# Optimization experiments

Hardware: AMD Instinct MI355X
Metric: run time of the kernel (lower is better)

The kernel has to match this reference:

```python
import jax, jax.numpy as jnp
import numpy as np

N_NODES = 50000
NEG_SLOPE = 0.2


def gat_conv(x, src, dst, W, att_src, att_dst, bias, concat):
    # x: [N, F_in], W: [H*D, F_in], att_*: [H, D], bias: [H*D] or [D]
    N = x.shape[0]
    H, D = att_src.shape
    h = (x @ W.T).reshape(N, H, D)                      # [N, H, D]
    a_src = jnp.einsum('nhd,hd->nh', h, att_src)        # [N, H]
    a_dst = jnp.einsum('nhd,hd->nh', h, att_dst)        # [N, H]
    e = jax.nn.leaky_relu(a_src[src] + a_dst[dst], NEG_SLOPE)  # [E, H]
    # softmax over incoming edges of each destination node
    m = jax.ops.segment_max(e, dst, num_segments=N)     # [N, H]
    ex = jnp.exp(e - m[dst])
    denom = jax.ops.segment_sum(ex, dst, num_segments=N)
    alpha = ex / denom[dst]                             # [E, H]
    msg = alpha[:, :, None] * h[src]                    # [E, H, D]
    out = jax.ops.segment_sum(msg, dst, num_segments=N) # [N, H, D]
    out = out.reshape(N, H * D) if concat else out.mean(axis=1)
    return out + bias


def setup_inputs() -> dict:
    key = jax.random.key(0)
    ks = jax.random.split(key, 10)
    nfeat, nhid, nclass, heads = 256, 128, 40, 4
    d1 = nhid // heads  # 32
    E = 800000
    x = jax.random.normal(ks[0], (N_NODES, nfeat), dtype=jnp.float32)
    edge_index = jax.random.randint(ks[1], (2, E), 0, N_NODES, dtype=jnp.int64)
    s = 0.1
    W1 = jax.random.normal(ks[2], (heads * d1, nfeat), dtype=jnp.float32) * s
    att_src1 = jax.random.normal(ks[3], (heads, d1), dtype=jnp.float32) * s
    att_dst1 = jax.random.normal(ks[4], (heads, d1), dtype=jnp.float32) * s
    b1 = jnp.zeros((heads * d1,), dtype=jnp.float32)
    W2 = jax.random.normal(ks[5], (nclass, nhid), dtype=jnp.float32) * s
    att_src2 = jax.random.normal(ks[6], (1, nclass), dtype=jnp.float32) * s
    att_dst2 = jax.random.normal(ks[7], (1, nclass), dtype=jnp.float32) * s
    b2 = jnp.zeros((nclass,), dtype=jnp.float32)
    return {"x": x, "edge_index": edge_index, "W1": W1, "att_src1": att_src1,
            "att_dst1": att_dst1, "b1": b1, "W2": W2, "att_src2": att_src2,
            "att_dst2": att_dst2, "b2": b2}


def reference(x, edge_index, W1, att_src1, att_dst1, b1, W2, att_src2, att_dst2, b2):
    # PyG GATConv adds self-loops by default
    loops = jnp.arange(N_NODES, dtype=edge_index.dtype)
    src = jnp.concatenate([edge_index[0], loops])
    dst = jnp.concatenate([edge_index[1], loops])
    h = gat_conv(x, src, dst, W1, att_src1, att_dst1, b1, concat=True)
    h = jax.nn.relu(h)
    # dropout is identity in eval mode
    out = gat_conv(h, src, dst, W2, att_src2, att_dst2, b2, concat=True)
    return out
```

## Files before the change

### kernel.cpp

```cpp
#include <hip/hip_runtime.h>
#include <hip/hip_bf16.h>
#include <cstdint>
#include <cstddef>

#define N_NODES 50000
#define NEG_SLOPE 0.2f
#define NB 196
#define BIN_CHUNK 8192
#define SLICE_MAX 14336

typedef float floatx4 __attribute__((ext_vector_type(4)));
typedef short shortx8 __attribute__((ext_vector_type(8)));

__device__ __forceinline__ unsigned short f2b(float f) {
    union { float f; unsigned u; } v; v.f = f;
    unsigned u = v.u;
    return (unsigned short)((u + 0x7FFFu + ((u >> 16) & 1u)) >> 16);
}
__device__ __forceinline__ float b2f(unsigned short b) {
    union { unsigned u; float f; } v; v.u = ((unsigned)b) << 16;
    return v.f;
}

__global__ __launch_bounds__(256) void bucket_hist_kernel(
    const int* __restrict__ ei, int E0, int E, int* __restrict__ bhist) {
    __shared__ int h[NB];
    int t = threadIdx.x;
    for (int i = t; i < NB; i += 256) h[i] = 0;
    __syncthreads();
    int base = blockIdx.x * BIN_CHUNK;
    int end = min(base + BIN_CHUNK, E);
    for (int e = base + t; e < end; e += 256) {
        int d = (e < E0) ? ei[E0 + e] : (e - E0);
        atomicAdd(&h[d >> 8], 1);
    }
    __syncthreads();
    for (int i = t; i < NB; i += 256)
        if (h[i]) atomicAdd(&bhist[i], h[i]);
}

__global__ __launch_bounds__(256) void bucket_scan_kernel(
    const int* __restrict__ bhist, int* __restrict__ bbase,
    int* __restrict__ bcursor, int* __restrict__ rowptr, int E) {
    __shared__ int buf[256];
    int t = threadIdx.x;
    int v = (t < NB) ? bhist[t] : 0;
    int x = v;
    for (int off = 1; off < 256; off <<= 1) {
        buf[t] = x; __syncthreads();
        int y = (t >= off) ? buf[t - off] : 0;
        __syncthreads();
        x += y;
    }
    if (t < NB) {
        bbase[t] = x - v;
        bcursor[t] = x - v;
    }
    if (t == NB - 1) bbase[NB] = x;
    if (t == 0) rowptr[N_NODES] = E;
}

__global__ __launch_bounds__(256) void bin_kernel(
    const int* __restrict__ ei, int E0, int E,
    int* __restrict__ bcursor, unsigned int* __restrict__ ebuf) {
    __shared__ int h[NB];
    __shared__ int gbase[NB];
    int t = threadIdx.x;
    for (int i = t; i < NB; i += 256) h[i] = 0;
    __syncthreads();
    int base = blockIdx.x * BIN_CHUNK;
    int end = min(base + BIN_CHUNK, E);
    for (int e = base + t; e < end; e += 256) {
        int d = (e < E0) ? ei[E0 + e] : (e - E0);
        atomicAdd(&h[d >> 8], 1);
    }
    __syncthreads();
    for (int i = t; i < NB; i += 256) {
        int c = h[i];
        gbase[i] = c ? atomicAdd(&bcursor[i], c) : 0;
        h[i] = 0;
    }
    __syncthreads();
    for (int e = base + t; e < end; e += 256) {
        int s, d;
        if (e < E0) { s = ei[e]; d = ei[E0 + e]; }
        else        { s = e - E0; d = e - E0; }
        int b = d >> 8;
        int off = atomicAdd(&h[b], 1);
        ebuf[gbase[b] + off] = (unsigned)s | ((unsigned)(d & 255) << 16);
    }
}

__global__ __launch_bounds__(256) void build_kernel(
    const unsigned int* __restrict__ ebuf, const int* __restrict__ bbase,
    int* __restrict__ rowptr, int* __restrict__ csr_src) {
    __shared__ int h[256];
    __shared__ int lrp[257];
    __shared__ int stag[SLICE_MAX];
    int b = blockIdx.x, t = threadIdx.x;
    int e0 = bbase[b], e1 = bbase[b + 1];
    int cnt = e1 - e0;
    int n0 = b << 8;
    h[t] = 0;
    __syncthreads();
    for (int i = t; i < cnt; i += 256)
        atomicAdd(&h[ebuf[e0 + i] >> 16], 1);
    __syncthreads();
    int v = h[t], x = v;
    __shared__ int buf[256];
    for (int off = 1; off < 256; off <<= 1) {
        buf[t] = x; __syncthreads();
        int y = (t >= off) ? buf[t - off] : 0;
        __syncthreads();
        x += y;
    }
    lrp[t] = x - v;
    if (t == 255) lrp[256] = x;
    h[t] = 0;
    __syncthreads();
    int n = n0 + t;
    if (n < N_NODES) rowptr[n] = e0 + lrp[t];
    for (int i = t; i < cnt; i += 256) {
        unsigned int v2 = ebuf[e0 + i];
        int dloc = v2 >> 16;
        int off = atomicAdd(&h[dloc], 1);
        stag[lrp[dloc] + off] = (int)(v2 & 0xFFFFu);
    }
    __syncthreads();
    for (int i = t; i < cnt; i += 256) csr_src[e0 + i] = stag[i];
}

template <int BM, int BN, int NREAL, int KK, typename InT>
__global__ __launch_bounds__(256) void gemm_bf16_kernel(
    const InT* __restrict__ A, const float* __restrict__ B,
    unsigned short* __restrict__ Cb, int M) {
    const int BK = 64, LDK = 72;
    const int NT = BN / 16;
    __shared__ unsigned short As[BM * LDK];
    __shared__ unsigned short Bs[BN * LDK];
    const int t = threadIdx.x;
    const int wave = t >> 6, lane = t & 63;
    const int lrow = lane & 15, lkg = lane >> 4;
    const int bm = blockIdx.x * BM;

    floatx4 acc[NT] = {};

    for (int k0 = 0; k0 < KK; k0 += BK) {
        __syncthreads();
        if constexpr (sizeof(InT) == 4) {
            for (int i = t; i < BM * 16; i += 256) {
                int r = i >> 4, c4 = (i & 15) << 2;
                int gr = bm + r;
                float4 v = make_float4(0.f, 0.f, 0.f, 0.f);
                if (gr < M) v = *(const float4*)&A[(size_t)gr * KK + k0 + c4];
                int o = r * LDK + c4;
                As[o] = f2b(v.x); As[o + 1] = f2b(v.y);
                As[o + 2] = f2b(v.z); As[o + 3] = f2b(v.w);
            }
        } else {
            for (int i = t; i < BM * 8; i += 256) {
                int r = i >> 3, c8 = (i & 7) << 3;
                int gr = bm + r;
                shortx8 v = {};
                if (gr < M) v = *(const shortx8*)&A[(size_t)gr * KK + k0 + c8];
                *(shortx8*)&As[r * LDK + c8] = v;
            }
        }
        for (int i = t; i < BN * 16; i += 256) {
            int r = i >> 4, c4 = (i & 15) << 2;
            float4 v = make_float4(0.f, 0.f, 0.f, 0.f);
            if (r < NREAL) v = *(const float4*)&B[(size_t)r * KK + k0 + c4];
            int o = r * LDK + c4;
            Bs[o] = f2b(v.x); Bs[o + 1] = f2b(v.y);
            Bs[o + 2] = f2b(v.z); Bs[o + 3] = f2b(v.w);
        }
        __syncthreads();

        for (int ks = 0; ks < BK; ks += 32) {
            int kc = ks + lkg * 8;
            int row = wave * 16 + lrow;
            shortx8 a = *(const shortx8*)&As[row * LDK + kc];
#pragma unroll
            for (int nt = 0; nt < NT; nt++) {
                shortx8 b = *(const shortx8*)&Bs[(nt * 16 + lrow) * LDK + kc];
                acc[nt] = __builtin_amdgcn_mfma_f32_16x16x32_bf16(a, b, acc[nt], 0, 0, 0);
            }
        }
    }
#pragma unroll
    for (int nt = 0; nt < NT; nt++)
#pragma unroll
        for (int r = 0; r < 4; r++) {
            int row = bm + wave * 16 + lkg * 4 + r;
            int col = nt * 16 + lrow;
            if (row < M && col < NREAL)
                Cb[(size_t)row * NREAL + col] = f2b(acc[nt][r]);
        }
}

__global__ void att1_kernel(const unsigned short* __restrict__ h1b,
                            const float* __restrict__ att_src,
                            const float* __restrict__ att_dst,
                            float* __restrict__ a_src, float* __restrict__ a_dst,
                            int N) {
    int i = blockIdx.x * blockDim.x + threadIdx.x;
    if (i >= N * 4) return;
    int h = i & 3;
    const ushort4* hp = (const ushort4*)(h1b + (size_t)i * 32);
    const float4* as = (const float4*)(att_src + h * 32);
    const float4* ad = (const float4*)(att_dst + h * 32);
    float ssum = 0.f, dsum = 0.f;
#pragma unroll
    for (int j = 0; j < 8; j++) {
        ushort4 hv = hp[j];
        float4 av = as[j], dv = ad[j];
        float x0 = b2f(hv.x), x1 = b2f(hv.y), x2 = b2f(hv.z), x3 = b2f(hv.w);
        ssum += x0 * av.x + x1 * av.y + x2 * av.z + x3 * av.w;
        dsum += x0 * dv.x + x1 * dv.y + x2 * dv.z + x3 * dv.w;
    }
    a_src[i] = ssum;
    a_dst[i] = dsum;
}

__global__ void att2_kernel(const unsigned short* __restrict__ h2b,
                            const float* __restrict__ att_src,
                            const float* __restrict__ att_dst,
                            float* __restrict__ a_src, float* __restrict__ a_dst,
                            int N) {
    int n = blockIdx.x * blockDim.x + threadIdx.x;
    if (n >= N) return;
    const ushort4* hp = (const ushort4*)(h2b + (size_t)n * 40);
    const float4* as = (const float4*)att_src;
    const float4* ad = (const float4*)att_dst;
    float ssum = 0.f, dsum = 0.f;
#pragma unroll
    for (int j = 0; j < 10; j++) {
        ushort4 hv = hp[j];
        float4 av = as[j], dv = ad[j];
        float x0 = b2f(hv.x), x1 = b2f(hv.y), x2 = b2f(hv.z), x3 = b2f(hv.w);
        ssum += x0 * av.x + x1 * av.y + x2 * av.z + x3 * av.w;
        dsum += x0 * dv.x + x1 * dv.y + x2 * dv.z + x3 * dv.w;
    }
    a_src[n] = ssum;
    a_dst[n] = dsum;
}

__global__ __launch_bounds__(256) void agg1_kernel(
    const unsigned short* __restrict__ h1b, const float* __restrict__ a_src,
    const float* __restrict__ a_dst, const int* __restrict__ rowptr,
    const int* __restrict__ csr_src, const float* __restrict__ b1,
    unsigned short* __restrict__ zb, int N) {
    int wave = threadIdx.x >> 6, lane = threadIdx.x & 63;
    int n = blockIdx.x * 4 + wave;
    if (n >= N) return;
    int half = lane >> 5, pos = lane & 31, head = pos >> 3;
    float adn = a_dst[n * 4 + (lane & 3)];
    int beg = rowptr[n], deg = rowptr[n + 1] - beg;

    floatx4 acc = {0.f, 0.f, 0.f, 0.f};
    float den = 0.f;
    for (int c0 = 0; c0 < deg; c0 += 16) {
        int idx = c0 + (lane >> 2);
        int s_e = (idx < deg) ? csr_src[beg + idx] : 0;
        float l = a_src[(s_e << 2) + (lane & 3)] + adn;
        l = l > 0.f ? l : NEG_SLOPE * l;
        float w_e = __expf(l);
        int cnt = min(16, deg - c0);
#pragma unroll
        for (int e = 0; e < 16; e += 2) {
            int el = e + half;
            int s = __shfl(s_e, el << 2);
            float w = __shfl(w_e, (el << 2) + head);
            if (el < cnt) {
                ushort4 v = *(const ushort4*)&h1b[(size_t)s * 128 + pos * 4];
                den += w;
                acc.x += w * b2f(v.x); acc.y += w * b2f(v.y);
                acc.z += w * b2f(v.z); acc.w += w * b2f(v.w);
            }
        }
    }
    acc.x += __shfl_xor(acc.x, 32);
    acc.y += __shfl_xor(acc.y, 32);
    acc.z += __shfl_xor(acc.z, 32);
    acc.w += __shfl_xor(acc.w, 32);
    den   += __shfl_xor(den, 32);
    if (half == 0) {
        float inv = 1.f / den;
        float4 bb = *(const float4*)&b1[pos * 4];
        float o0 = fmaxf(acc.x * inv + bb.x, 0.f);
        float o1 = fmaxf(acc.y * inv + bb.y, 0.f);
        float o2 = fmaxf(acc.z * inv + bb.z, 0.f);
        float o3 = fmaxf(acc.w * inv + bb.w, 0.f);
        ushort4 r;
        r.x = f2b(o0); r.y = f2b(o1); r.z = f2b(o2); r.w = f2b(o3);
        *(ushort4*)&zb[(size_t)n * 128 + pos * 4] = r;
    }
}

__global__ __launch_bounds__(256) void agg2_kernel(
    const unsigned short* __restrict__ h2b, const float* __restrict__ a_src,
    const float* __restrict__ a_dst, const int* __restrict__ rowptr,
    const int* __restrict__ csr_src, const float* __restrict__ b2,
    float* __restrict__ out, int N) {
    int wave = threadIdx.x >> 6, lane = threadIdx.x & 63;
    int n = blockIdx.x * 4 + wave;
    if (n >= N) return;
    int half = lane >> 5, pos = lane & 31;
    float adn = a_dst[n];
    int beg = rowptr[n], deg = rowptr[n + 1] - beg;

    float2 acc = {0.f, 0.f};
    float den = 0.f;
    for (int c0 = 0; c0 < deg; c0 += 32) {
        int idx = c0 + lane;
        int s_e = (idx < deg) ? csr_src[beg + idx] : 0;
        float l = a_src[s_e] + adn;
        l = l > 0.f ? l : NEG_SLOPE * l;
        float w_e = __expf(l);
        int cnt = min(32, deg - c0);
#pragma unroll
        for (int e = 0; e < 32; e += 2) {
            int el = e + half;
            int s = __shfl(s_e, el);
            float w = __shfl(w_e, el);
            if (el < cnt) {
                den += w;
                if (pos < 20) {
                    ushort2 v = *(const ushort2*)&h2b[(size_t)s * 40 + pos * 2];
                    acc.x += w * b2f(v.x);
                    acc.y += w * b2f(v.y);
                }
            }
        }
    }
    acc.x += __shfl_xor(acc.x, 32);
    acc.y += __shfl_xor(acc.y, 32);
    den   += __shfl_xor(den, 32);
    if (half == 0 && pos < 20) {
        float inv = 1.f / den;
        float2 bb = *(const float2*)&b2[pos * 2];
        float2 o;
        o.x = acc.x * inv + bb.x;
        o.y = acc.y * inv + bb.y;
        *(float2*)&out[(size_t)n * 40 + pos * 2] = o;
    }
}

extern "C" void kernel_launch(void* const* d_in, const int* in_sizes, int n_in,
                              void* d_out, int out_size, void* d_ws, size_t ws_size,
                              hipStream_t stream) {
    const float* x        = (const float*)d_in[0];
    const int*   ei       = (const int*)d_in[1];
    const float* W1       = (const float*)d_in[2];
    const float* att_src1 = (const float*)d_in[3];
    const float* att_dst1 = (const float*)d_in[4];
    const float* b1       = (const float*)d_in[5];
    const float* W2       = (const float*)d_in[6];
    const float* att_src2 = (const float*)d_in[7];
    const float* att_dst2 = (const float*)d_in[8];
    const float* b2       = (const float*)d_in[9];
    float* out = (float*)d_out;

    const int N  = N_NODES;
    const int E0 = in_sizes[1] / 2;
    const int E  = E0 + N;
    const int NBLK = (E + BIN_CHUNK - 1) / BIN_CHUNK;

    char* ws = (char*)d_ws;
    unsigned short* h1b = (unsigned short*)(ws + 0);
    unsigned short* zb  = (unsigned short*)(ws + 12800000);
    unsigned short* h2b = (unsigned short*)(ws + 25600000);
    float* a_src1 = (float*)(ws + 29600000);
    float* a_dst1 = (float*)(ws + 30400000);
    float* a_src2 = (float*)(ws + 31200000);
    float* a_dst2 = (float*)(ws + 31400000);
    int*   rowptr = (int*)(ws + 31600000);
    int*   bhist  = (int*)(ws + 31800192);
    int*   bbase  = (int*)(ws + 31801088);
    int*   bcursor= (int*)(ws + 31801984);
    unsigned int* ebuf = (unsigned int*)(ws + 31802880);
    int*   csr_src= (int*)(ws + 35202880);

    hipMemsetAsync(bhist, 0, NB * sizeof(int), stream);

    bucket_hist_kernel<<<NBLK, 256, 0, stream>>>(ei, E0, E, bhist);
    bucket_scan_kernel<<<1, 256, 0, stream>>>(bhist, bbase, bcursor, rowptr, E);
    bin_kernel<<<NBLK, 256, 0, stream>>>(ei, E0, E, bcursor, ebuf);
    build_kernel<<<NB, 256, 0, stream>>>(ebuf, bbase, rowptr, csr_src);

    gemm_bf16_kernel<64, 128, 128, 256, float>
        <<<(N + 63) / 64, 256, 0, stream>>>(x, W1, h1b, N);
    att1_kernel<<<(N * 4 + 255) / 256, 256, 0, stream>>>(h1b, att_src1, att_dst1, a_src1, a_dst1, N);
    agg1_kernel<<<(N + 3) / 4, 256, 0, stream>>>(h1b, a_src1, a_dst1, rowptr, csr_src, b1, zb, N);

    gemm_bf16_kernel<64, 48, 40, 128, unsigned short>
        <<<(N + 63) / 64, 256, 0, stream>>>(zb, W2, h2b, N);
    att2_kernel<<<(N + 255) / 256, 256, 0, stream>>>(h2b, att_src2, att_dst2, a_src2, a_dst2, N);
    agg2_kernel<<<(N + 3) / 4, 256, 0, stream>>>(h2b, a_src2, a_dst2, rowptr, csr_src, b2, out, N);
}
```

Before: 267.1 us.

## Widen per-lane gathers and batch loads in both GAT aggregation kernels

In layer 1, each lane now loads 8 bf16 features (16 bytes) instead of 4, so one wave processes 4 edges at once, and the index and weight shuffles are batched ahead of the loads so several gathers are in flight together. In layer 2, three 20-lane groups process three edges at once instead of two 32-lane halves, which uses 60 of 64 lanes instead of 40. Loads are batched in groups of four, and out-of-range edge weights are zeroed so padded edges add nothing. The change aims to raise memory-level parallelism and lane utilisation in the gather-bound aggregation, at the cost of more registers and a more involved cross-lane reduction.

```diff
diff --git a/kernel.cpp b/kernel.cpp
--- a/kernel.cpp
+++ b/kernel.cpp
@@ -253,47 +253,67 @@
     int wave = threadIdx.x >> 6, lane = threadIdx.x & 63;
     int n = blockIdx.x * 4 + wave;
     if (n >= N) return;
-    int half = lane >> 5, pos = lane & 31, head = pos >> 3;
+    int eg = lane >> 4;
+    int fpos = lane & 15;
+    int hd = fpos >> 2;
     float adn = a_dst[n * 4 + (lane & 3)];
     int beg = rowptr[n], deg = rowptr[n + 1] - beg;
 
-    floatx4 acc = {0.f, 0.f, 0.f, 0.f};
+    float acc[8] = {0.f, 0.f, 0.f, 0.f, 0.f, 0.f, 0.f, 0.f};
     float den = 0.f;
     for (int c0 = 0; c0 < deg; c0 += 16) {
         int idx = c0 + (lane >> 2);
         int s_e = (idx < deg) ? csr_src[beg + idx] : 0;
         float l = a_src[(s_e << 2) + (lane & 3)] + adn;
         l = l > 0.f ? l : NEG_SLOPE * l;
-        float w_e = __expf(l);
+        float w_e = (idx < deg) ? __expf(l) : 0.f;
         int cnt = min(16, deg - c0);
-#pragma unroll
-        for (int e = 0; e < 16; e += 2) {
-            int el = e + half;
-            int s = __shfl(s_e, el << 2);
-            float w = __shfl(w_e, (el << 2) + head);
-            if (el < cnt) {
-                ushort4 v = *(const ushort4*)&h1b[(size_t)s * 128 + pos * 4];
+        int s4[4]; float w4[4]; shortx8 v4[4];
+#pragma unroll
+        for (int q = 0; q < 4; q++) {
+            if (q * 4 < cnt) {
+                int el = (q << 2) + eg;
+                s4[q] = __shfl(s_e, el << 2);
+                w4[q] = __shfl(w_e, (el << 2) + hd);
+            }
+        }
+#pragma unroll
+        for (int q = 0; q < 4; q++) {
+            if (q * 4 < cnt)
+                v4[q] = *(const shortx8*)&h1b[(size_t)s4[q] * 128 + fpos * 8];
+        }
+#pragma unroll
+        for (int q = 0; q < 4; q++) {
+            if (q * 4 < cnt) {
+                float w = w4[q];
                 den += w;
-                acc.x += w * b2f(v.x); acc.y += w * b2f(v.y);
-                acc.z += w * b2f(v.z); acc.w += w * b2f(v.w);
-            }
-        }
-    }
-    acc.x += __shfl_xor(acc.x, 32);
-    acc.y += __shfl_xor(acc.y, 32);
-    acc.z += __shfl_xor(acc.z, 32);
-    acc.w += __shfl_xor(acc.w, 32);
-    den   += __shfl_xor(den, 32);
-    if (half == 0) {
+#pragma unroll
+                for (int j = 0; j < 8; j++)
+                    acc[j] += w * b2f((unsigned short)v4[q][j]);
+            }
+        }
+    }
+#pragma unroll
+    for (int j = 0; j < 8; j++) {
+        acc[j] += __shfl_xor(acc[j], 16);
+        acc[j] += __shfl_xor(acc[j], 32);
+    }
+    den += __shfl_xor(den, 16);
+    den += __shfl_xor(den, 32);
+    if (lane < 16) {
         float inv = 1.f / den;
-        float4 bb = *(const float4*)&b1[pos * 4];
-        float o0 = fmaxf(acc.x * inv + bb.x, 0.f);
-        float o1 = fmaxf(acc.y * inv + bb.y, 0.f);
-        float o2 = fmaxf(acc.z * inv + bb.z, 0.f);
-        float o3 = fmaxf(acc.w * inv + bb.w, 0.f);
-        ushort4 r;
-        r.x = f2b(o0); r.y = f2b(o1); r.z = f2b(o2); r.w = f2b(o3);
-        *(ushort4*)&zb[(size_t)n * 128 + pos * 4] = r;
+        float4 bb0 = *(const float4*)&b1[fpos * 8];
+        float4 bb1 = *(const float4*)&b1[fpos * 8 + 4];
+        shortx8 r;
+        r[0] = (short)f2b(fmaxf(acc[0] * inv + bb0.x, 0.f));
+        r[1] = (short)f2b(fmaxf(acc[1] * inv + bb0.y, 0.f));
+        r[2] = (short)f2b(fmaxf(acc[2] * inv + bb0.z, 0.f));
+        r[3] = (short)f2b(fmaxf(acc[3] * inv + bb0.w, 0.f));
+        r[4] = (short)f2b(fmaxf(acc[4] * inv + bb1.x, 0.f));
+        r[5] = (short)f2b(fmaxf(acc[5] * inv + bb1.y, 0.f));
+        r[6] = (short)f2b(fmaxf(acc[6] * inv + bb1.z, 0.f));
+        r[7] = (short)f2b(fmaxf(acc[7] * inv + bb1.w, 0.f));
+        *(shortx8*)&zb[(size_t)n * 128 + fpos * 8] = r;
     }
 }
 
@@ -305,44 +325,62 @@
     int wave = threadIdx.x >> 6, lane = threadIdx.x & 63;
     int n = blockIdx.x * 4 + wave;
     if (n >= N) return;
-    int half = lane >> 5, pos = lane & 31;
+    int eg = (lane >= 40) ? 2 : (lane >= 20 ? 1 : 0);
+    int fp = lane - eg * 20;
+    bool act = fp < 20;
     float adn = a_dst[n];
     int beg = rowptr[n], deg = rowptr[n + 1] - beg;
 
     float2 acc = {0.f, 0.f};
     float den = 0.f;
-    for (int c0 = 0; c0 < deg; c0 += 32) {
+    for (int c0 = 0; c0 < deg; c0 += 48) {
         int idx = c0 + lane;
-        int s_e = (idx < deg) ? csr_src[beg + idx] : 0;
+        bool cv = (lane < 48) && (idx < deg);
+        int s_e = cv ? csr_src[beg + idx] : 0;
         float l = a_src[s_e] + adn;
         l = l > 0.f ? l : NEG_SLOPE * l;
-        float w_e = __expf(l);
-        int cnt = min(32, deg - c0);
-#pragma unroll
-        for (int e = 0; e < 32; e += 2) {
-            int el = e + half;
-            int s = __shfl(s_e, el);
-            float w = __shfl(w_e, el);
-            if (el < cnt) {
-                den += w;
-                if (pos < 20) {
-                    ushort2 v = *(const ushort2*)&h2b[(size_t)s * 40 + pos * 2];
-                    acc.x += w * b2f(v.x);
-                    acc.y += w * b2f(v.y);
+        float w_e = cv ? __expf(l) : 0.f;
+        int cnt = min(48, deg - c0);
+#pragma unroll
+        for (int qq = 0; qq < 4; qq++) {
+            if (qq * 12 < cnt) {
+                int s4[4]; float w4[4]; ushort2 v4[4];
+#pragma unroll
+                for (int q = 0; q < 4; q++) {
+                    int el = qq * 12 + q * 3 + eg;
+                    s4[q] = __shfl(s_e, el);
+                    w4[q] = __shfl(w_e, el);
                 }
-            }
-        }
-    }
-    acc.x += __shfl_xor(acc.x, 32);
-    acc.y += __shfl_xor(acc.y, 32);
-    den   += __shfl_xor(den, 32);
-    if (half == 0 && pos < 20) {
-        float inv = 1.f / den;
-        float2 bb = *(const float2*)&b2[pos * 2];
+#pragma unroll
+                for (int q = 0; q < 4; q++) {
+                    if (act)
+                        v4[q] = *(const ushort2*)&h2b[(size_t)s4[q] * 40 + fp * 2];
+                }
+#pragma unroll
+                for (int q = 0; q < 4; q++) {
+                    float w = w4[q];
+                    den += w;
+                    if (act) {
+                        acc.x += w * b2f(v4[q].x);
+                        acc.y += w * b2f(v4[q].y);
+                    }
+                }
+            }
+        }
+    }
+    float a1x = __shfl(acc.x, fp + 20), a2x = __shfl(acc.x, fp + 40);
+    float a1y = __shfl(acc.y, fp + 20), a2y = __shfl(acc.y, fp + 40);
+    float d1  = __shfl(den,  fp + 20), d2  = __shfl(den,  fp + 40);
+    if (lane < 20) {
+        float sx = acc.x + a1x + a2x;
+        float sy = acc.y + a1y + a2y;
+        float dtot = den + d1 + d2;
+        float inv = 1.f / dtot;
+        float2 bb = *(const float2*)&b2[fp * 2];
         float2 o;
-        o.x = acc.x * inv + bb.x;
-        o.y = acc.y * inv + bb.y;
-        *(float2*)&out[(size_t)n * 40 + pos * 2] = o;
+        o.x = sx * inv + bb.x;
+        o.y = sy * inv + bb.y;
+        *(float2*)&out[(size_t)n * 40 + fp * 2] = o;
     }
 }
 
```

Measured after the change: 244.0 us. 1.09x faster.
